# Kernel optimization log

Measured on AMD Instinct MI355X. Metric: run time of the kernel, lower is better.

## Reference

```python
import jax, jax.numpy as jnp
import numpy as np

EPS = 1e-12  # torch F.normalize eps


def _pairwise_sqdist(x, y):
    # P[b,i,j] = |x_i|^2 + |y_j|^2 - 2 x_i.y_j  (matches batch_pairwise_dist)
    rx = jnp.sum(x * x, axis=-1)[:, :, None]          # [B,N,1]
    ry = jnp.sum(y * y, axis=-1)[:, None, :]          # [B,1,M]
    zz = jnp.einsum('bnd,bmd->bnm', x, y)             # [B,N,M]
    return rx + ry - 2.0 * zz


def _unit_axis1(t):
    # torch F.normalize(t, dim=1): L2-normalize across the edge dimension (axis=1)
    n = jnp.sqrt(jnp.sum(t * t, axis=1, keepdims=True))
    return t / jnp.maximum(n, EPS)


def setup_inputs() -> dict:
    key = jax.random.key(0)
    k1, k2, k3, k4 = jax.random.split(key, 4)
    B, N, E = 2, 8192, 24576
    gts = jax.random.normal(k1, (B, N, 6), dtype=jnp.float32)
    preds = jax.random.normal(k2, (B, N, 6), dtype=jnp.float32)
    gts_normals = jax.random.normal(k3, (B, N, 3), dtype=jnp.float32)
    sphere_edges = jax.random.randint(k4, (E, 2), 0, N, dtype=jnp.int32)
    return {"gts": gts, "preds": preds, "gts_normals": gts_normals,
            "sphere_edges": sphere_edges}


def reference(gts, preds, gts_normals, sphere_edges):
    gts_points = gts[:, :, :3]
    preds_points = preds[:, :, :3]
    gts_colors = gts[:, :, 3:]
    preds_colors = preds[:, :, 3:]
    e0 = sphere_edges[:, 0]
    e1 = sphere_edges[:, 1]

    # ---- edge loss ----
    edge = preds_points[:, e0, :] - preds_points[:, e1, :]      # [B,E,3]
    edge_length = jnp.sum(jnp.abs(edge), axis=2)                # [B,E]
    edge_loss = jnp.sum(jnp.mean(edge_length, axis=1)) * 300.0

    # ---- color chamfer loss ----
    Pc = _pairwise_sqdist(gts_colors, preds_colors)             # [B,N,M]
    color_loss = jnp.sum(jnp.min(Pc, axis=1)) + jnp.sum(jnp.min(Pc, axis=2))

    # ---- point chamfer loss ----
    P = _pairwise_sqdist(gts_points, preds_points)              # [B,N,M]
    dist_f2s = jnp.min(P, axis=1)                               # [B,M]
    dist_s2f = jnp.min(P, axis=2)                               # [B,N]
    idx_s2f = jnp.argmin(P, axis=2)                             # [B,N] (into M)
    champfer_loss = (jnp.sum(jnp.mean(dist_f2s, axis=1))
                     + jnp.sum(jnp.mean(dist_s2f, axis=1)) * 0.55) * 3000.0

    # ---- normal loss ----
    # gather gts_normals by nearest-pred index (valid since N == M), then by edge start
    normal = jnp.take_along_axis(gts_normals, idx_s2f[:, :, None], axis=1)  # [B,N,3]
    normal = normal[:, e0, :]                                   # [B,E,3]
    # original casts edge to Long then back to float -> truncation toward zero
    edge_t = jnp.trunc(edge)
    cosine = jnp.abs(jnp.sum(_unit_axis1(normal) * _unit_axis1(edge_t), axis=2))
    normal_loss = jnp.sum(jnp.mean(cosine, axis=1)) * 0.5

    return color_loss + edge_loss + champfer_loss + normal_loss
```

## Files before the change

### kernel.cpp

```cpp
#include <hip/hip_runtime.h>
#include <stdint.h>

#define TPB 256
#define ROWS_PB 256
#define TC 256
#define CS 8
#define FINAL_BLOCKS 64

typedef unsigned long long u64;
typedef unsigned int u32;

__device__ __forceinline__ float waveReduceSum(float v){
#pragma unroll
  for (int o = 32; o > 0; o >>= 1) v += __shfl_down(v, o, 64);
  return v;
}

__device__ __forceinline__ float blockReduceSum(float v, float* buf){
  v = waveReduceSum(v);
  __syncthreads();
  if ((threadIdx.x & 63) == 0) buf[threadIdx.x >> 6] = v;
  __syncthreads();
  return buf[0] + buf[1] + buf[2] + buf[3];
}

template<bool NEED_IDX>
__device__ __forceinline__ void pass_body(
    const float* __restrict__ rows, const float* __restrict__ cols,
    void* __restrict__ outPackV, u32* __restrict__ outCol, int N, int cpc)
{
  __shared__ float4 ptsT[TC];
  __shared__ float4 colT[TC];
  __shared__ u64 mPack[4 * TPB];
  __shared__ u32 mCol[4 * TPB];

  const int b = blockIdx.y;
  const int rb = blockIdx.x / CS;
  const int chunk = blockIdx.x - rb * CS;
  const int t = threadIdx.x;
  const int lane = t & 63;
  const int w = t >> 6;
  const int rowBase = rb * ROWS_PB;
  const int colBase = chunk * cpc;

  float ax[4], ay[4], az[4], rx[4];
  float cr[4], cg[4], cbl[4], rc[4];
  float bD[4], bC[4];
  int bM[4];
#pragma unroll
  for (int k = 0; k < 4; k++){
    const float* p = rows + ((size_t)b * N + (rowBase + lane + 64 * k)) * 6;
    float p0 = p[0], p1 = p[1], p2 = p[2], p3 = p[3], p4 = p[4], p5 = p[5];
    ax[k] = -2.f * p0; ay[k] = -2.f * p1; az[k] = -2.f * p2;
    rx[k] = fmaf(p0, p0, fmaf(p1, p1, p2 * p2));
    cr[k] = -2.f * p3; cg[k] = -2.f * p4; cbl[k] = -2.f * p5;
    rc[k] = fmaf(p3, p3, fmaf(p4, p4, p5 * p5));
    bD[k] = 3.4e38f; bC[k] = 3.4e38f; bM[k] = 0;
  }

  for (int tb = 0; tb < cpc; tb += TC){
    const float* p = cols + ((size_t)b * N + (colBase + tb + t)) * 6;
    float q0 = p[0], q1 = p[1], q2 = p[2], q3 = p[3], q4 = p[4], q5 = p[5];
    ptsT[t] = make_float4(q0, q1, q2, fmaf(q0, q0, fmaf(q1, q1, q2 * q2)));
    colT[t] = make_float4(q3, q4, q5, fmaf(q3, q3, fmaf(q4, q4, q5 * q5)));
    __syncthreads();
#pragma unroll 4
    for (int j = 0; j < TC / 4; j += 2){
      const int mlA = j * 4 + w;
      const int mlB = mlA + 4;
      const float4 pA = ptsT[mlA], pB = ptsT[mlB];
      const float4 cA = colT[mlA], cB = colT[mlB];
      const int gA = colBase + tb + mlA;
      const int gB = gA + 4;
#pragma unroll
      for (int k = 0; k < 4; k++){
        float tA = fmaf(ax[k], pA.x, fmaf(ay[k], pA.y, fmaf(az[k], pA.z, pA.w)));
        float tB = fmaf(ax[k], pB.x, fmaf(ay[k], pB.y, fmaf(az[k], pB.z, pB.w)));
        if (NEED_IDX){
          if (tA < bD[k]) { bD[k] = tA; bM[k] = gA; }
          if (tB < bD[k]) { bD[k] = tB; bM[k] = gB; }
        } else {
          bD[k] = fminf(fminf(tA, tB), bD[k]);
        }
        float eA = fmaf(cr[k], cA.x, fmaf(cg[k], cA.y, fmaf(cbl[k], cA.z, cA.w)));
        float eB = fmaf(cr[k], cB.x, fmaf(cg[k], cB.y, fmaf(cbl[k], cB.z, cB.w)));
        bC[k] = fminf(fminf(eA, eB), bC[k]);
      }
    }
    __syncthreads();
  }

#pragma unroll
  for (int k = 0; k < 4; k++){
    int r = lane + 64 * k;
    float dv = fmaxf(bD[k] + rx[k], 0.f);
    float cv = fmaxf(bC[k] + rc[k], 0.f);
    mPack[w * TPB + r] = NEED_IDX
        ? (((u64)__float_as_uint(dv) << 32) | (u32)bM[k])
        : (u64)__float_as_uint(dv);
    mCol[w * TPB + r] = __float_as_uint(cv);
  }
  __syncthreads();
  u64 pk = mPack[t];
  u32 cm = mCol[t];
#pragma unroll
  for (int i = 1; i < 4; i++){
    u64 p2 = mPack[i * TPB + t]; if (p2 < pk) pk = p2;
    u32 c2 = mCol[i * TPB + t];  if (c2 < cm) cm = c2;
  }
  size_t g = (size_t)b * N + rowBase + t;
  if (NEED_IDX) atomicMin((u64*)outPackV + g, pk);
  else          atomicMin((u32*)outPackV + g, (u32)pk);
  atomicMin(&outCol[g], cm);
}

__global__ void __launch_bounds__(TPB) pass_all(
    const float* __restrict__ gts, const float* __restrict__ preds,
    u64* __restrict__ packS2F, u32* __restrict__ colMin2,
    u32* __restrict__ distF2S, u32* __restrict__ colMin1, int N, int cpc)
{
  if (blockIdx.z == 0) pass_body<true >(gts,  preds, packS2F, colMin2, N, cpc);
  else                 pass_body<false>(preds, gts,  distF2S, colMin1, N, cpc);
}

__global__ void __launch_bounds__(TPB) edge_pass1(
    const float* __restrict__ preds, const float* __restrict__ normals,
    const int* __restrict__ edges, const u64* __restrict__ packS2F,
    float* __restrict__ acc, int N, int E)
{
  __shared__ float buf[7][4];
  int gid = blockIdx.x * TPB + threadIdx.x;
  int b = gid / E, e = gid - b * E;
  int e0 = edges[2 * e], e1 = edges[2 * e + 1];
  const float* p0 = preds + ((size_t)b * N + e0) * 6;
  const float* p1 = preds + ((size_t)b * N + e1) * 6;
  float ex = p0[0] - p1[0], ey = p0[1] - p1[1], ez = p0[2] - p1[2];
  u32 idx = (u32)packS2F[(size_t)b * N + e0];
  const float* nr = normals + ((size_t)b * N + idx) * 3;
  float n0 = nr[0], n1 = nr[1], n2 = nr[2];
  float t0 = truncf(ex), t1 = truncf(ey), t2 = truncf(ez);
  float v[7] = { fabsf(ex) + fabsf(ey) + fabsf(ez),
                 n0 * n0, n1 * n1, n2 * n2, t0 * t0, t1 * t1, t2 * t2 };
  int lane = threadIdx.x & 63, w = threadIdx.x >> 6;
#pragma unroll
  for (int q = 0; q < 7; q++){
    float s = waveReduceSum(v[q]);
    if (lane == 0) buf[q][w] = s;
  }
  __syncthreads();
  if (threadIdx.x < 7){
    int q = threadIdx.x;
    float s = buf[q][0] + buf[q][1] + buf[q][2] + buf[q][3];
    int off = (q == 0) ? 0 : (q < 4 ? 1 + b * 3 + (q - 1) : 7 + b * 3 + (q - 4));
    atomicAdd(&acc[off], s);
  }
}

__global__ void __launch_bounds__(TPB) edge2_and_sum(
    const float* __restrict__ preds, const float* __restrict__ normals,
    const int* __restrict__ edges, const u64* __restrict__ packS2F,
    const u32* __restrict__ distF2S, const u32* __restrict__ colMin2,
    const u32* __restrict__ colMin1, float* __restrict__ acc,
    int N, int E, int BNtot, int nEdge)
{
  __shared__ float buf[4];
  if ((int)blockIdx.x < nEdge){
    int gid = blockIdx.x * TPB + threadIdx.x;
    int b = gid / E, e = gid - b * E;
    int e0 = edges[2 * e], e1 = edges[2 * e + 1];
    const float* p0 = preds + ((size_t)b * N + e0) * 6;
    const float* p1 = preds + ((size_t)b * N + e1) * 6;
    float ex = p0[0] - p1[0], ey = p0[1] - p1[1], ez = p0[2] - p1[2];
    u32 idx = (u32)packS2F[(size_t)b * N + e0];
    const float* nr = normals + ((size_t)b * N + idx) * 3;
    float t0 = truncf(ex), t1 = truncf(ey), t2 = truncf(ez);
    float r0 = 1.0f / (fmaxf(sqrtf(acc[1 + b * 3 + 0]), 1e-12f) * fmaxf(sqrtf(acc[7 + b * 3 + 0]), 1e-12f));
    float r1 = 1.0f / (fmaxf(sqrtf(acc[1 + b * 3 + 1]), 1e-12f) * fmaxf(sqrtf(acc[7 + b * 3 + 1]), 1e-12f));
    float r2 = 1.0f / (fmaxf(sqrtf(acc[1 + b * 3 + 2]), 1e-12f) * fmaxf(sqrtf(acc[7 + b * 3 + 2]), 1e-12f));
    float cosv = fabsf(nr[0] * t0 * r0 + nr[1] * t1 * r1 + nr[2] * t2 * r2);
    float s = blockReduceSum(cosv, buf);
    if (threadIdx.x == 0) atomicAdd(&acc[13], s);
  } else {
    int sb = blockIdx.x - nEdge;
    float invN = 1.0f / (float)N;
    float s = 0.f;
    for (int i = sb * TPB + threadIdx.x; i < BNtot; i += FINAL_BLOCKS * TPB){
      float s2f = __uint_as_float((u32)(packS2F[i] >> 32));
      float f2s = __uint_as_float(distF2S[i]);
      s += 3000.0f * invN * f2s + 1650.0f * invN * s2f
         + __uint_as_float(colMin1[i]) + __uint_as_float(colMin2[i]);
    }
    s = blockReduceSum(s, buf);
    if (threadIdx.x == 0) atomicAdd(&acc[14], s);
  }
}

__global__ void combine_kernel(const float* __restrict__ acc,
                               float* __restrict__ out, int E)
{
  out[0] = acc[14] + acc[0] * (300.0f / (float)E) + acc[13] * (0.5f / (float)E);
}

extern "C" void kernel_launch(void* const* d_in, const int* in_sizes, int n_in,
                              void* d_out, int out_size, void* d_ws, size_t ws_size,
                              hipStream_t stream)
{
  const float* gts     = (const float*)d_in[0];
  const float* preds   = (const float*)d_in[1];
  const float* normals = (const float*)d_in[2];
  const int*   edges   = (const int*)d_in[3];

  const int B = 2;
  const int BNtot = in_sizes[2] / 3;
  const int N = BNtot / B;
  const int E = in_sizes[3] / 2;

  char* ws = (char*)d_ws;
  u64* packS2F = (u64*)ws;
  u32* distF2S = (u32*)(ws + (size_t)BNtot * 8);
  u32* colMin2 = (u32*)(ws + (size_t)BNtot * 12);
  u32* colMin1 = (u32*)(ws + (size_t)BNtot * 16);
  float* acc   = (float*)(ws + (size_t)BNtot * 20);

  hipMemsetAsync(ws, 0xFF, (size_t)BNtot * 20, stream);
  hipMemsetAsync(acc, 0, 64, stream);

  int cpc = N / CS;
  dim3 gp((N / ROWS_PB) * CS, B, 2);
  pass_all<<<gp, TPB, 0, stream>>>(gts, preds, packS2F, colMin2, distF2S, colMin1, N, cpc);

  int nEdge = (B * E) / TPB;
  edge_pass1<<<nEdge, TPB, 0, stream>>>(preds, normals, edges, packS2F, acc, N, E);
  edge2_and_sum<<<nEdge + FINAL_BLOCKS, TPB, 0, stream>>>(
      preds, normals, edges, packS2F, distF2S, colMin2, colMin1, acc, N, E, BNtot, nEdge);
  combine_kernel<<<1, 1, 0, stream>>>(acc, (float*)d_out, E);
}
```

Baseline: 119.0 us.

## Replace atomicMin reductions with per-chunk partials and fuse edge stages

The pairwise pass now writes per-column-chunk partial minima to separate buffers instead of using global atomicMin, which removes the large 0xFF memset. A mid kernel reduces the partials and computes the chamfer sums and normal norms. The edge-length and trunc-norm sums are folded into the pass kernel as extra blocks. The combine kernel is replaced by a last-block-done finish in the cosine kernel. The column split is doubled and LDS is aliased to raise occupancy, at the cost of more partial-buffer traffic and repeated CS-way gathers per edge.

```diff
diff --git a/kernel.cpp b/kernel.cpp
--- a/kernel.cpp
+++ b/kernel.cpp
@@ -4,8 +4,7 @@
 #define TPB 256
 #define ROWS_PB 256
 #define TC 256
-#define CS 8
-#define FINAL_BLOCKS 64
+#define CS 16
 
 typedef unsigned long long u64;
 typedef unsigned int u32;
@@ -16,23 +15,24 @@
   return v;
 }
 
-__device__ __forceinline__ float blockReduceSum(float v, float* buf){
+__device__ __forceinline__ float blockReduceSum(float v, float* buf4){
   v = waveReduceSum(v);
   __syncthreads();
-  if ((threadIdx.x & 63) == 0) buf[threadIdx.x >> 6] = v;
+  if ((threadIdx.x & 63) == 0) buf4[threadIdx.x >> 6] = v;
   __syncthreads();
-  return buf[0] + buf[1] + buf[2] + buf[3];
+  return buf4[0] + buf4[1] + buf4[2] + buf4[3];
 }
 
 template<bool NEED_IDX>
 __device__ __forceinline__ void pass_body(
     const float* __restrict__ rows, const float* __restrict__ cols,
-    void* __restrict__ outPackV, u32* __restrict__ outCol, int N, int cpc)
-{
-  __shared__ float4 ptsT[TC];
-  __shared__ float4 colT[TC];
-  __shared__ u64 mPack[4 * TPB];
-  __shared__ u32 mCol[4 * TPB];
+    void* __restrict__ outPart, u32* __restrict__ outColPart,
+    char* lds, int N, int cpc, int BNtot)
+{
+  float4* ptsT = (float4*)lds;
+  float4* colT = (float4*)(lds + 4096);
+  u64* mPack   = (u64*)lds;
+  u32* mCol    = (u32*)(lds + 8192);
 
   const int b = blockIdx.y;
   const int rb = blockIdx.x / CS;
@@ -108,97 +108,131 @@
     u64 p2 = mPack[i * TPB + t]; if (p2 < pk) pk = p2;
     u32 c2 = mCol[i * TPB + t];  if (c2 < cm) cm = c2;
   }
-  size_t g = (size_t)b * N + rowBase + t;
-  if (NEED_IDX) atomicMin((u64*)outPackV + g, pk);
-  else          atomicMin((u32*)outPackV + g, (u32)pk);
-  atomicMin(&outCol[g], cm);
-}
-
-__global__ void __launch_bounds__(TPB) pass_all(
+  size_t g = (size_t)chunk * BNtot + (size_t)b * N + rowBase + t;
+  if (NEED_IDX) ((u64*)outPart)[g] = pk;
+  else          ((u32*)outPart)[g] = (u32)pk;
+  outColPart[g] = cm;
+}
+
+__device__ __forceinline__ void edge_partial(
+    const float* __restrict__ preds, const int* __restrict__ edges,
+    float* __restrict__ acc, int N, int E, int NXB)
+{
+  __shared__ float ebuf[4];
+  int e = ((int)blockIdx.x - NXB) * TPB + threadIdx.x;
+  int b = blockIdx.y;
+  int e0 = edges[2 * e], e1 = edges[2 * e + 1];
+  const float* p0 = preds + ((size_t)b * N + e0) * 6;
+  const float* p1 = preds + ((size_t)b * N + e1) * 6;
+  float ex = p0[0] - p1[0], ey = p0[1] - p1[1], ez = p0[2] - p1[2];
+  float t0 = truncf(ex), t1 = truncf(ey), t2 = truncf(ez);
+  float v[4] = { fabsf(ex) + fabsf(ey) + fabsf(ez), t0 * t0, t1 * t1, t2 * t2 };
+#pragma unroll
+  for (int q = 0; q < 4; q++){
+    float s = blockReduceSum(v[q], ebuf);
+    if (threadIdx.x == 0) atomicAdd(&acc[q == 0 ? 0 : 7 + b * 3 + (q - 1)], s);
+  }
+}
+
+__global__ void __launch_bounds__(TPB, 8) pass_all(
     const float* __restrict__ gts, const float* __restrict__ preds,
-    u64* __restrict__ packS2F, u32* __restrict__ colMin2,
-    u32* __restrict__ distF2S, u32* __restrict__ colMin1, int N, int cpc)
-{
-  if (blockIdx.z == 0) pass_body<true >(gts,  preds, packS2F, colMin2, N, cpc);
-  else                 pass_body<false>(preds, gts,  distF2S, colMin1, N, cpc);
-}
-
-__global__ void __launch_bounds__(TPB) edge_pass1(
+    const int* __restrict__ edges,
+    u64* __restrict__ packPart, u32* __restrict__ distPart,
+    u32* __restrict__ colPart2, u32* __restrict__ colPart1,
+    float* __restrict__ acc, int N, int cpc, int NXB, int E, int BNtot)
+{
+  __shared__ __align__(16) char lds[12288];
+  if ((int)blockIdx.x >= NXB){
+    if (blockIdx.z == 0) edge_partial(preds, edges, acc, N, E, NXB);
+    return;
+  }
+  if (blockIdx.z == 0) pass_body<true >(gts,  preds, packPart, colPart2, lds, N, cpc, BNtot);
+  else                 pass_body<false>(preds, gts,  distPart, colPart1, lds, N, cpc, BNtot);
+}
+
+__global__ void __launch_bounds__(TPB) mid_kernel(
+    const u64* __restrict__ packPart, const u32* __restrict__ distPart,
+    const u32* __restrict__ colPart2, const u32* __restrict__ colPart1,
+    const float* __restrict__ normals, const int* __restrict__ edges,
+    float* __restrict__ acc, int N, int E, int BNtot, int nRowBlk)
+{
+  __shared__ float buf4[4];
+  if ((int)blockIdx.x < nRowBlk){
+    int row = blockIdx.x * TPB + threadIdx.x;
+    u64 pk = packPart[row];
+    u32 f2 = distPart[row], c2 = colPart2[row], c1 = colPart1[row];
+#pragma unroll
+    for (int c = 1; c < CS; c++){
+      size_t o = (size_t)c * BNtot + row;
+      u64 p = packPart[o]; if (p < pk) pk = p;
+      u32 d = distPart[o]; if (d < f2) f2 = d;
+      u32 x2 = colPart2[o]; if (x2 < c2) c2 = x2;
+      u32 x1 = colPart1[o]; if (x1 < c1) c1 = x1;
+    }
+    float invN = 1.f / (float)N;
+    float s = 3000.f * invN * __uint_as_float(f2)
+            + 1650.f * invN * __uint_as_float((u32)(pk >> 32))
+            + __uint_as_float(c1) + __uint_as_float(c2);
+    s = blockReduceSum(s, buf4);
+    if (threadIdx.x == 0) atomicAdd(&acc[14], s);
+  } else {
+    int gid = ((int)blockIdx.x - nRowBlk) * TPB + threadIdx.x;
+    int b = gid / E, e = gid - b * E;
+    int e0 = edges[2 * e];
+    size_t r = (size_t)b * N + e0;
+    u64 pk = packPart[r];
+#pragma unroll
+    for (int c = 1; c < CS; c++){
+      u64 p = packPart[(size_t)c * BNtot + r]; if (p < pk) pk = p;
+    }
+    const float* nr = normals + ((size_t)b * N + (u32)pk) * 3;
+    float n0 = nr[0], n1 = nr[1], n2 = nr[2];
+    float s0 = blockReduceSum(n0 * n0, buf4);
+    if (threadIdx.x == 0) atomicAdd(&acc[1 + b * 3 + 0], s0);
+    float s1 = blockReduceSum(n1 * n1, buf4);
+    if (threadIdx.x == 0) atomicAdd(&acc[1 + b * 3 + 1], s1);
+    float s2 = blockReduceSum(n2 * n2, buf4);
+    if (threadIdx.x == 0) atomicAdd(&acc[1 + b * 3 + 2], s2);
+  }
+}
+
+__global__ void __launch_bounds__(TPB) edge_cos_kernel(
     const float* __restrict__ preds, const float* __restrict__ normals,
-    const int* __restrict__ edges, const u64* __restrict__ packS2F,
-    float* __restrict__ acc, int N, int E)
-{
-  __shared__ float buf[7][4];
+    const int* __restrict__ edges, const u64* __restrict__ packPart,
+    float* __restrict__ acc, float* __restrict__ out,
+    int N, int E, int BNtot, int nBlocks)
+{
+  __shared__ float buf4[4];
   int gid = blockIdx.x * TPB + threadIdx.x;
   int b = gid / E, e = gid - b * E;
   int e0 = edges[2 * e], e1 = edges[2 * e + 1];
   const float* p0 = preds + ((size_t)b * N + e0) * 6;
   const float* p1 = preds + ((size_t)b * N + e1) * 6;
   float ex = p0[0] - p1[0], ey = p0[1] - p1[1], ez = p0[2] - p1[2];
-  u32 idx = (u32)packS2F[(size_t)b * N + e0];
-  const float* nr = normals + ((size_t)b * N + idx) * 3;
-  float n0 = nr[0], n1 = nr[1], n2 = nr[2];
   float t0 = truncf(ex), t1 = truncf(ey), t2 = truncf(ez);
-  float v[7] = { fabsf(ex) + fabsf(ey) + fabsf(ez),
-                 n0 * n0, n1 * n1, n2 * n2, t0 * t0, t1 * t1, t2 * t2 };
-  int lane = threadIdx.x & 63, w = threadIdx.x >> 6;
-#pragma unroll
-  for (int q = 0; q < 7; q++){
-    float s = waveReduceSum(v[q]);
-    if (lane == 0) buf[q][w] = s;
-  }
-  __syncthreads();
-  if (threadIdx.x < 7){
-    int q = threadIdx.x;
-    float s = buf[q][0] + buf[q][1] + buf[q][2] + buf[q][3];
-    int off = (q == 0) ? 0 : (q < 4 ? 1 + b * 3 + (q - 1) : 7 + b * 3 + (q - 4));
-    atomicAdd(&acc[off], s);
-  }
-}
-
-__global__ void __launch_bounds__(TPB) edge2_and_sum(
-    const float* __restrict__ preds, const float* __restrict__ normals,
-    const int* __restrict__ edges, const u64* __restrict__ packS2F,
-    const u32* __restrict__ distF2S, const u32* __restrict__ colMin2,
-    const u32* __restrict__ colMin1, float* __restrict__ acc,
-    int N, int E, int BNtot, int nEdge)
-{
-  __shared__ float buf[4];
-  if ((int)blockIdx.x < nEdge){
-    int gid = blockIdx.x * TPB + threadIdx.x;
-    int b = gid / E, e = gid - b * E;
-    int e0 = edges[2 * e], e1 = edges[2 * e + 1];
-    const float* p0 = preds + ((size_t)b * N + e0) * 6;
-    const float* p1 = preds + ((size_t)b * N + e1) * 6;
-    float ex = p0[0] - p1[0], ey = p0[1] - p1[1], ez = p0[2] - p1[2];
-    u32 idx = (u32)packS2F[(size_t)b * N + e0];
-    const float* nr = normals + ((size_t)b * N + idx) * 3;
-    float t0 = truncf(ex), t1 = truncf(ey), t2 = truncf(ez);
-    float r0 = 1.0f / (fmaxf(sqrtf(acc[1 + b * 3 + 0]), 1e-12f) * fmaxf(sqrtf(acc[7 + b * 3 + 0]), 1e-12f));
-    float r1 = 1.0f / (fmaxf(sqrtf(acc[1 + b * 3 + 1]), 1e-12f) * fmaxf(sqrtf(acc[7 + b * 3 + 1]), 1e-12f));
-    float r2 = 1.0f / (fmaxf(sqrtf(acc[1 + b * 3 + 2]), 1e-12f) * fmaxf(sqrtf(acc[7 + b * 3 + 2]), 1e-12f));
-    float cosv = fabsf(nr[0] * t0 * r0 + nr[1] * t1 * r1 + nr[2] * t2 * r2);
-    float s = blockReduceSum(cosv, buf);
-    if (threadIdx.x == 0) atomicAdd(&acc[13], s);
-  } else {
-    int sb = blockIdx.x - nEdge;
-    float invN = 1.0f / (float)N;
-    float s = 0.f;
-    for (int i = sb * TPB + threadIdx.x; i < BNtot; i += FINAL_BLOCKS * TPB){
-      float s2f = __uint_as_float((u32)(packS2F[i] >> 32));
-      float f2s = __uint_as_float(distF2S[i]);
-      s += 3000.0f * invN * f2s + 1650.0f * invN * s2f
-         + __uint_as_float(colMin1[i]) + __uint_as_float(colMin2[i]);
-    }
-    s = blockReduceSum(s, buf);
-    if (threadIdx.x == 0) atomicAdd(&acc[14], s);
-  }
-}
-
-__global__ void combine_kernel(const float* __restrict__ acc,
-                               float* __restrict__ out, int E)
-{
-  out[0] = acc[14] + acc[0] * (300.0f / (float)E) + acc[13] * (0.5f / (float)E);
+  size_t r = (size_t)b * N + e0;
+  u64 pk = packPart[r];
+#pragma unroll
+  for (int c = 1; c < CS; c++){
+    u64 p = packPart[(size_t)c * BNtot + r]; if (p < pk) pk = p;
+  }
+  const float* nr = normals + ((size_t)b * N + (u32)pk) * 3;
+  float r0 = 1.f / (fmaxf(sqrtf(acc[1 + b * 3 + 0]), 1e-12f) * fmaxf(sqrtf(acc[7 + b * 3 + 0]), 1e-12f));
+  float r1 = 1.f / (fmaxf(sqrtf(acc[1 + b * 3 + 1]), 1e-12f) * fmaxf(sqrtf(acc[7 + b * 3 + 1]), 1e-12f));
+  float r2 = 1.f / (fmaxf(sqrtf(acc[1 + b * 3 + 2]), 1e-12f) * fmaxf(sqrtf(acc[7 + b * 3 + 2]), 1e-12f));
+  float cosv = fabsf(nr[0] * t0 * r0 + nr[1] * t1 * r1 + nr[2] * t2 * r2);
+  float s = blockReduceSum(cosv, buf4);
+  if (threadIdx.x == 0){
+    atomicAdd(&acc[13], s);
+    __threadfence();
+    u32 old = atomicAdd((u32*)&acc[15], 1u);
+    if (old == (u32)(nBlocks - 1)){
+      float a0  = atomicAdd(&acc[0],  0.f);
+      float a13 = atomicAdd(&acc[13], 0.f);
+      float a14 = atomicAdd(&acc[14], 0.f);
+      out[0] = a14 + a0 * (300.f / (float)E) + a13 * (0.5f / (float)E);
+    }
+  }
 }
 
 extern "C" void kernel_launch(void* const* d_in, const int* in_sizes, int n_in,
@@ -216,22 +250,28 @@
   const int E = in_sizes[3] / 2;
 
   char* ws = (char*)d_ws;
-  u64* packS2F = (u64*)ws;
-  u32* distF2S = (u32*)(ws + (size_t)BNtot * 8);
-  u32* colMin2 = (u32*)(ws + (size_t)BNtot * 12);
-  u32* colMin1 = (u32*)(ws + (size_t)BNtot * 16);
-  float* acc   = (float*)(ws + (size_t)BNtot * 20);
-
-  hipMemsetAsync(ws, 0xFF, (size_t)BNtot * 20, stream);
+  size_t nPart = (size_t)CS * BNtot;
+  u64* packPart = (u64*)ws;
+  u32* distPart = (u32*)(ws + nPart * 8);
+  u32* colPart2 = (u32*)(ws + nPart * 12);
+  u32* colPart1 = (u32*)(ws + nPart * 16);
+  float* acc    = (float*)(ws + nPart * 20);
+
   hipMemsetAsync(acc, 0, 64, stream);
 
   int cpc = N / CS;
-  dim3 gp((N / ROWS_PB) * CS, B, 2);
-  pass_all<<<gp, TPB, 0, stream>>>(gts, preds, packS2F, colMin2, distF2S, colMin1, N, cpc);
-
-  int nEdge = (B * E) / TPB;
-  edge_pass1<<<nEdge, TPB, 0, stream>>>(preds, normals, edges, packS2F, acc, N, E);
-  edge2_and_sum<<<nEdge + FINAL_BLOCKS, TPB, 0, stream>>>(
-      preds, normals, edges, packS2F, distF2S, colMin2, colMin1, acc, N, E, BNtot, nEdge);
-  combine_kernel<<<1, 1, 0, stream>>>(acc, (float*)d_out, E);
-}
+  int NXB = (N / ROWS_PB) * CS;
+  int nEdgeBlk = (B * E) / (TPB * B);
+  dim3 gp(NXB + nEdgeBlk, B, 2);
+  pass_all<<<gp, TPB, 0, stream>>>(gts, preds, edges, packPart, distPart,
+                                   colPart2, colPart1, acc, N, cpc, NXB, E, BNtot);
+
+  int nRowBlk = BNtot / TPB;
+  int nMid = nRowBlk + (B * E) / TPB;
+  mid_kernel<<<nMid, TPB, 0, stream>>>(packPart, distPart, colPart2, colPart1,
+                                       normals, edges, acc, N, E, BNtot, nRowBlk);
+
+  int nCos = (B * E) / TPB;
+  edge_cos_kernel<<<nCos, TPB, 0, stream>>>(preds, normals, edges, packPart,
+                                            acc, (float*)d_out, N, E, BNtot, nCos);
+}
```

Result: slower. 146.4 us (+23.0%).

## Fuse all stages into one cooperative kernel and pack argmin index into distance bits

Applied to the files above, without the earlier changes.

Merges the chamfer pass, the edge and row reductions, and the final combine into a single cooperative kernel separated by grid-wide syncs. A last-block counter writes the output, so the extra launches and the combine kernel go away. The pass also works on 8 rows per thread with finer column chunks for more register reuse. The nearest-neighbour index is stored in the low 13 mantissa bits of the distance, so a plain fminf replaces the compare-and-select. That truncates the s2f distances slightly. A three-launch fallback runs if the cooperative launch fails.

```diff
diff --git a/kernel.cpp b/kernel.cpp
--- a/kernel.cpp
+++ b/kernel.cpp
@@ -1,11 +1,16 @@
 #include <hip/hip_runtime.h>
+#include <hip/hip_cooperative_groups.h>
 #include <stdint.h>
 
+namespace cgrp = cooperative_groups;
+
 #define TPB 256
-#define ROWS_PB 256
+#define ROWS_PB 512
+#define KROWS 8
 #define TC 256
-#define CS 8
-#define FINAL_BLOCKS 64
+#define CS 16
+#define IDXMASK 0x1FFFu
+#define HIMASK  0xFFFFE000u
 
 typedef unsigned long long u64;
 typedef unsigned int u32;
@@ -16,47 +21,42 @@
   return v;
 }
 
-__device__ __forceinline__ float blockReduceSum(float v, float* buf){
+__device__ __forceinline__ float blockReduceSum(float v, float* buf4){
   v = waveReduceSum(v);
   __syncthreads();
-  if ((threadIdx.x & 63) == 0) buf[threadIdx.x >> 6] = v;
+  if ((threadIdx.x & 63) == 0) buf4[threadIdx.x >> 6] = v;
   __syncthreads();
-  return buf[0] + buf[1] + buf[2] + buf[3];
+  return buf4[0] + buf4[1] + buf4[2] + buf4[3];
 }
 
 template<bool NEED_IDX>
-__device__ __forceinline__ void pass_body(
+__device__ __forceinline__ void pass_phase(
     const float* __restrict__ rows, const float* __restrict__ cols,
-    void* __restrict__ outPackV, u32* __restrict__ outCol, int N, int cpc)
+    u64* __restrict__ outPack, u32* __restrict__ outDist, u32* __restrict__ outCol,
+    int N, int cpc, int b, int rb, int chunk,
+    float4* ptsT, float4* colT, u64* mPack, u32* mCol)
 {
-  __shared__ float4 ptsT[TC];
-  __shared__ float4 colT[TC];
-  __shared__ u64 mPack[4 * TPB];
-  __shared__ u32 mCol[4 * TPB];
-
-  const int b = blockIdx.y;
-  const int rb = blockIdx.x / CS;
-  const int chunk = blockIdx.x - rb * CS;
   const int t = threadIdx.x;
   const int lane = t & 63;
   const int w = t >> 6;
   const int rowBase = rb * ROWS_PB;
   const int colBase = chunk * cpc;
 
-  float ax[4], ay[4], az[4], rx[4];
-  float cr[4], cg[4], cbl[4], rc[4];
-  float bD[4], bC[4];
-  int bM[4];
-#pragma unroll
-  for (int k = 0; k < 4; k++){
+  float ax[KROWS], ay[KROWS], az[KROWS], rx[KROWS];
+  float cr[KROWS], cg_[KROWS], cb[KROWS], rc[KROWS];
+  float bD[KROWS], bC[KROWS];
+#pragma unroll
+  for (int k = 0; k < KROWS; k++){
     const float* p = rows + ((size_t)b * N + (rowBase + lane + 64 * k)) * 6;
     float p0 = p[0], p1 = p[1], p2 = p[2], p3 = p[3], p4 = p[4], p5 = p[5];
     ax[k] = -2.f * p0; ay[k] = -2.f * p1; az[k] = -2.f * p2;
     rx[k] = fmaf(p0, p0, fmaf(p1, p1, p2 * p2));
-    cr[k] = -2.f * p3; cg[k] = -2.f * p4; cbl[k] = -2.f * p5;
+    cr[k] = -2.f * p3; cg_[k] = -2.f * p4; cb[k] = -2.f * p5;
     rc[k] = fmaf(p3, p3, fmaf(p4, p4, p5 * p5));
-    bD[k] = 3.4e38f; bC[k] = 3.4e38f; bM[k] = 0;
-  }
+    bD[k] = 3.4e38f; bC[k] = 3.4e38f;
+  }
+  mPack[t] = ~0ull; mPack[t + TPB] = ~0ull;
+  mCol[t] = 0xFFFFFFFFu; mCol[t + TPB] = 0xFFFFFFFFu;
 
   for (int tb = 0; tb < cpc; tb += TC){
     const float* p = cols + ((size_t)b * N + (colBase + tb + t)) * 6;
@@ -66,24 +66,24 @@
     __syncthreads();
 #pragma unroll 4
     for (int j = 0; j < TC / 4; j += 2){
-      const int mlA = j * 4 + w;
-      const int mlB = mlA + 4;
+      const int mlA = j * 4 + w, mlB = mlA + 4;
       const float4 pA = ptsT[mlA], pB = ptsT[mlB];
       const float4 cA = colT[mlA], cB = colT[mlB];
-      const int gA = colBase + tb + mlA;
-      const int gB = gA + 4;
-#pragma unroll
-      for (int k = 0; k < 4; k++){
+      const u32 gA = (u32)(colBase + tb + mlA);
+      const u32 gB = gA + 4;
+#pragma unroll
+      for (int k = 0; k < KROWS; k++){
         float tA = fmaf(ax[k], pA.x, fmaf(ay[k], pA.y, fmaf(az[k], pA.z, pA.w)));
         float tB = fmaf(ax[k], pB.x, fmaf(ay[k], pB.y, fmaf(az[k], pB.z, pB.w)));
         if (NEED_IDX){
-          if (tA < bD[k]) { bD[k] = tA; bM[k] = gA; }
-          if (tB < bD[k]) { bD[k] = tB; bM[k] = gB; }
+          float pkA = __uint_as_float((__float_as_uint(tA) & HIMASK) | gA);
+          float pkB = __uint_as_float((__float_as_uint(tB) & HIMASK) | gB);
+          bD[k] = fminf(fminf(pkA, pkB), bD[k]);
         } else {
           bD[k] = fminf(fminf(tA, tB), bD[k]);
         }
-        float eA = fmaf(cr[k], cA.x, fmaf(cg[k], cA.y, fmaf(cbl[k], cA.z, cA.w)));
-        float eB = fmaf(cr[k], cB.x, fmaf(cg[k], cB.y, fmaf(cbl[k], cB.z, cB.w)));
+        float eA = fmaf(cr[k], cA.x, fmaf(cg_[k], cA.y, fmaf(cb[k], cA.z, cA.w)));
+        float eB = fmaf(cr[k], cB.x, fmaf(cg_[k], cB.y, fmaf(cb[k], cB.z, cB.w)));
         bC[k] = fminf(fminf(eA, eB), bC[k]);
       }
     }
@@ -91,81 +91,107 @@
   }
 
 #pragma unroll
-  for (int k = 0; k < 4; k++){
+  for (int k = 0; k < KROWS; k++){
     int r = lane + 64 * k;
-    float dv = fmaxf(bD[k] + rx[k], 0.f);
+    u32 db = __float_as_uint(bD[k]);
+    float dv; u32 idx = 0;
+    if (NEED_IDX){ idx = db & IDXMASK; dv = __uint_as_float(db & HIMASK) + rx[k]; }
+    else { dv = bD[k] + rx[k]; }
+    dv = fmaxf(dv, 0.f);
     float cv = fmaxf(bC[k] + rc[k], 0.f);
-    mPack[w * TPB + r] = NEED_IDX
-        ? (((u64)__float_as_uint(dv) << 32) | (u32)bM[k])
-        : (u64)__float_as_uint(dv);
-    mCol[w * TPB + r] = __float_as_uint(cv);
+    atomicMin(&mPack[r], ((u64)__float_as_uint(dv) << 32) | idx);
+    atomicMin(&mCol[r], __float_as_uint(cv));
   }
   __syncthreads();
-  u64 pk = mPack[t];
-  u32 cm = mCol[t];
-#pragma unroll
-  for (int i = 1; i < 4; i++){
-    u64 p2 = mPack[i * TPB + t]; if (p2 < pk) pk = p2;
-    u32 c2 = mCol[i * TPB + t];  if (c2 < cm) cm = c2;
-  }
-  size_t g = (size_t)b * N + rowBase + t;
-  if (NEED_IDX) atomicMin((u64*)outPackV + g, pk);
-  else          atomicMin((u32*)outPackV + g, (u32)pk);
-  atomicMin(&outCol[g], cm);
-}
-
-__global__ void __launch_bounds__(TPB) pass_all(
+#pragma unroll
+  for (int i = 0; i < ROWS_PB; i += TPB){
+    int r = t + i;
+    size_t g = (size_t)b * N + rowBase + r;
+    u64 pk = mPack[r]; u32 cm = mCol[r];
+    if (NEED_IDX) atomicMin(&outPack[g], pk);
+    else          atomicMin(&outDist[g], (u32)(pk >> 32));
+    atomicMin(&outCol[g], cm);
+  }
+}
+
+__global__ void __launch_bounds__(TPB, 4) combined(
     const float* __restrict__ gts, const float* __restrict__ preds,
-    u64* __restrict__ packS2F, u32* __restrict__ colMin2,
-    u32* __restrict__ distF2S, u32* __restrict__ colMin1, int N, int cpc)
+    const float* __restrict__ normals, const int* __restrict__ edges,
+    u64* __restrict__ packS2F, u32* __restrict__ distF2S,
+    u32* __restrict__ colMin2, u32* __restrict__ colMin1,
+    float* __restrict__ acc, float* __restrict__ out,
+    int N, int E, int cpc, int nRowBlk, int nEdgeBlk, int mode)
 {
-  if (blockIdx.z == 0) pass_body<true >(gts,  preds, packS2F, colMin2, N, cpc);
-  else                 pass_body<false>(preds, gts,  distF2S, colMin1, N, cpc);
-}
-
-__global__ void __launch_bounds__(TPB) edge_pass1(
-    const float* __restrict__ preds, const float* __restrict__ normals,
-    const int* __restrict__ edges, const u64* __restrict__ packS2F,
-    float* __restrict__ acc, int N, int E)
-{
-  __shared__ float buf[7][4];
-  int gid = blockIdx.x * TPB + threadIdx.x;
-  int b = gid / E, e = gid - b * E;
-  int e0 = edges[2 * e], e1 = edges[2 * e + 1];
-  const float* p0 = preds + ((size_t)b * N + e0) * 6;
-  const float* p1 = preds + ((size_t)b * N + e1) * 6;
-  float ex = p0[0] - p1[0], ey = p0[1] - p1[1], ez = p0[2] - p1[2];
-  u32 idx = (u32)packS2F[(size_t)b * N + e0];
-  const float* nr = normals + ((size_t)b * N + idx) * 3;
-  float n0 = nr[0], n1 = nr[1], n2 = nr[2];
-  float t0 = truncf(ex), t1 = truncf(ey), t2 = truncf(ez);
-  float v[7] = { fabsf(ex) + fabsf(ey) + fabsf(ez),
-                 n0 * n0, n1 * n1, n2 * n2, t0 * t0, t1 * t1, t2 * t2 };
-  int lane = threadIdx.x & 63, w = threadIdx.x >> 6;
-#pragma unroll
-  for (int q = 0; q < 7; q++){
-    float s = waveReduceSum(v[q]);
-    if (lane == 0) buf[q][w] = s;
-  }
-  __syncthreads();
-  if (threadIdx.x < 7){
-    int q = threadIdx.x;
-    float s = buf[q][0] + buf[q][1] + buf[q][2] + buf[q][3];
-    int off = (q == 0) ? 0 : (q < 4 ? 1 + b * 3 + (q - 1) : 7 + b * 3 + (q - 4));
-    atomicAdd(&acc[off], s);
-  }
-}
-
-__global__ void __launch_bounds__(TPB) edge2_and_sum(
-    const float* __restrict__ preds, const float* __restrict__ normals,
-    const int* __restrict__ edges, const u64* __restrict__ packS2F,
-    const u32* __restrict__ distF2S, const u32* __restrict__ colMin2,
-    const u32* __restrict__ colMin1, float* __restrict__ acc,
-    int N, int E, int BNtot, int nEdge)
-{
-  __shared__ float buf[4];
-  if ((int)blockIdx.x < nEdge){
-    int gid = blockIdx.x * TPB + threadIdx.x;
+  __shared__ float4 ptsT[TC];
+  __shared__ float4 colT[TC];
+  __shared__ u64 mPack[ROWS_PB];
+  __shared__ u32 mCol[ROWS_PB];
+  __shared__ float red4[4];
+  __shared__ float buf7[7][4];
+  __shared__ float chn[3];
+
+  const int x = (int)blockIdx.x;
+  const int t = threadIdx.x;
+
+  if (mode <= 1){
+    int perDB = (N / ROWS_PB) * CS;
+    int dir = x / (2 * perDB);
+    int rem = x - dir * 2 * perDB;
+    int b = rem / perDB;
+    int id = rem - b * perDB;
+    int rb = id / CS;
+    int chunk = id - rb * CS;
+    if (dir == 0) pass_phase<true >(gts,  preds, packS2F, distF2S, colMin2,
+                                    N, cpc, b, rb, chunk, ptsT, colT, mPack, mCol);
+    else          pass_phase<false>(preds, gts,  packS2F, distF2S, colMin1,
+                                    N, cpc, b, rb, chunk, ptsT, colT, mPack, mCol);
+    if (mode == 1) return;
+  }
+  if (mode == 0) cgrp::this_grid().sync();
+
+  if (mode == 0 || mode == 2){
+    if (x < nRowBlk){
+      int row = x * TPB + t;
+      u64 pk = packS2F[row];
+      float invN = 1.f / (float)N;
+      float s = 3000.f * invN * __uint_as_float(distF2S[row])
+              + 1650.f * invN * __uint_as_float((u32)(pk >> 32))
+              + __uint_as_float(colMin1[row]) + __uint_as_float(colMin2[row]);
+      s = blockReduceSum(s, red4);
+      if (t == 0) atomicAdd(&acc[14], s);
+    } else if (x < nRowBlk + nEdgeBlk){
+      int gid = (x - nRowBlk) * TPB + t;
+      int b = gid / E, e = gid - b * E;
+      int e0 = edges[2 * e], e1 = edges[2 * e + 1];
+      const float* p0 = preds + ((size_t)b * N + e0) * 6;
+      const float* p1 = preds + ((size_t)b * N + e1) * 6;
+      float ex = p0[0] - p1[0], ey = p0[1] - p1[1], ez = p0[2] - p1[2];
+      u32 idx = (u32)packS2F[(size_t)b * N + e0];
+      const float* nr = normals + ((size_t)b * N + idx) * 3;
+      float n0 = nr[0], n1 = nr[1], n2 = nr[2];
+      float t0 = truncf(ex), t1 = truncf(ey), t2 = truncf(ez);
+      float v[7] = { fabsf(ex) + fabsf(ey) + fabsf(ez),
+                     n0 * n0, n1 * n1, n2 * n2, t0 * t0, t1 * t1, t2 * t2 };
+      int lane = t & 63, w = t >> 6;
+#pragma unroll
+      for (int q = 0; q < 7; q++){
+        float s = waveReduceSum(v[q]);
+        if (lane == 0) buf7[q][w] = s;
+      }
+      __syncthreads();
+      if (t < 7){
+        float s = buf7[t][0] + buf7[t][1] + buf7[t][2] + buf7[t][3];
+        int off = (t == 0) ? 0 : ((t < 4) ? (1 + b * 3 + t - 1) : (7 + b * 3 + t - 4));
+        atomicAdd(&acc[off], s);
+      }
+    }
+    if (mode == 2) return;
+  }
+  if (mode == 0) cgrp::this_grid().sync();
+
+  int xe = (mode == 3) ? x : x - nRowBlk;
+  if (xe >= 0 && xe < nEdgeBlk){
+    int gid = xe * TPB + t;
     int b = gid / E, e = gid - b * E;
     int e0 = edges[2 * e], e1 = edges[2 * e + 1];
     const float* p0 = preds + ((size_t)b * N + e0) * 6;
@@ -174,31 +200,29 @@
     u32 idx = (u32)packS2F[(size_t)b * N + e0];
     const float* nr = normals + ((size_t)b * N + idx) * 3;
     float t0 = truncf(ex), t1 = truncf(ey), t2 = truncf(ez);
-    float r0 = 1.0f / (fmaxf(sqrtf(acc[1 + b * 3 + 0]), 1e-12f) * fmaxf(sqrtf(acc[7 + b * 3 + 0]), 1e-12f));
-    float r1 = 1.0f / (fmaxf(sqrtf(acc[1 + b * 3 + 1]), 1e-12f) * fmaxf(sqrtf(acc[7 + b * 3 + 1]), 1e-12f));
-    float r2 = 1.0f / (fmaxf(sqrtf(acc[1 + b * 3 + 2]), 1e-12f) * fmaxf(sqrtf(acc[7 + b * 3 + 2]), 1e-12f));
-    float cosv = fabsf(nr[0] * t0 * r0 + nr[1] * t1 * r1 + nr[2] * t2 * r2);
-    float s = blockReduceSum(cosv, buf);
-    if (threadIdx.x == 0) atomicAdd(&acc[13], s);
-  } else {
-    int sb = blockIdx.x - nEdge;
-    float invN = 1.0f / (float)N;
-    float s = 0.f;
-    for (int i = sb * TPB + threadIdx.x; i < BNtot; i += FINAL_BLOCKS * TPB){
-      float s2f = __uint_as_float((u32)(packS2F[i] >> 32));
-      float f2s = __uint_as_float(distF2S[i]);
-      s += 3000.0f * invN * f2s + 1650.0f * invN * s2f
-         + __uint_as_float(colMin1[i]) + __uint_as_float(colMin2[i]);
-    }
-    s = blockReduceSum(s, buf);
-    if (threadIdx.x == 0) atomicAdd(&acc[14], s);
-  }
-}
-
-__global__ void combine_kernel(const float* __restrict__ acc,
-                               float* __restrict__ out, int E)
-{
-  out[0] = acc[14] + acc[0] * (300.0f / (float)E) + acc[13] * (0.5f / (float)E);
+    if (t == 0){
+#pragma unroll
+      for (int c = 0; c < 3; c++){
+        float Sn = atomicAdd(&acc[1 + b * 3 + c], 0.f);
+        float Se = atomicAdd(&acc[7 + b * 3 + c], 0.f);
+        chn[c] = 1.f / (fmaxf(sqrtf(Sn), 1e-12f) * fmaxf(sqrtf(Se), 1e-12f));
+      }
+    }
+    __syncthreads();
+    float cosv = fabsf(nr[0] * t0 * chn[0] + nr[1] * t1 * chn[1] + nr[2] * t2 * chn[2]);
+    float s = blockReduceSum(cosv, red4);
+    if (t == 0){
+      atomicAdd(&acc[13], s);
+      __threadfence();
+      u32 old = atomicAdd((u32*)&acc[15], 1u);
+      if (old == (u32)(nEdgeBlk - 1)){
+        float a0  = atomicAdd(&acc[0],  0.f);
+        float a13 = atomicAdd(&acc[13], 0.f);
+        float a14 = atomicAdd(&acc[14], 0.f);
+        out[0] = a14 + a0 * (300.f / (float)E) + a13 * (0.5f / (float)E);
+      }
+    }
+  }
 }
 
 extern "C" void kernel_launch(void* const* d_in, const int* in_sizes, int n_in,
@@ -226,12 +250,27 @@
   hipMemsetAsync(acc, 0, 64, stream);
 
   int cpc = N / CS;
-  dim3 gp((N / ROWS_PB) * CS, B, 2);
-  pass_all<<<gp, TPB, 0, stream>>>(gts, preds, packS2F, colMin2, distF2S, colMin1, N, cpc);
-
-  int nEdge = (B * E) / TPB;
-  edge_pass1<<<nEdge, TPB, 0, stream>>>(preds, normals, edges, packS2F, acc, N, E);
-  edge2_and_sum<<<nEdge + FINAL_BLOCKS, TPB, 0, stream>>>(
-      preds, normals, edges, packS2F, distF2S, colMin2, colMin1, acc, N, E, BNtot, nEdge);
-  combine_kernel<<<1, 1, 0, stream>>>(acc, (float*)d_out, E);
-}
+  int nPass = 2 * B * (N / ROWS_PB) * CS;
+  int nRowBlk = BNtot / TPB;
+  int nEdgeBlk = (B * E) / TPB;
+  float* outp = (float*)d_out;
+
+  int mode0 = 0;
+  void* args[] = { (void*)&gts, (void*)&preds, (void*)&normals, (void*)&edges,
+                   (void*)&packS2F, (void*)&distF2S, (void*)&colMin2, (void*)&colMin1,
+                   (void*)&acc, (void*)&outp, (void*)&N, (void*)&E, (void*)&cpc,
+                   (void*)&nRowBlk, (void*)&nEdgeBlk, (void*)&mode0 };
+  hipError_t err = hipLaunchCooperativeKernel((const void*)combined,
+                                              dim3(nPass), dim3(TPB), args, 0, stream);
+  if (err != hipSuccess){
+    combined<<<nPass, TPB, 0, stream>>>(gts, preds, normals, edges, packS2F, distF2S,
+                                        colMin2, colMin1, acc, outp, N, E, cpc,
+                                        nRowBlk, nEdgeBlk, 1);
+    combined<<<nRowBlk + nEdgeBlk, TPB, 0, stream>>>(gts, preds, normals, edges, packS2F,
+                                        distF2S, colMin2, colMin1, acc, outp, N, E, cpc,
+                                        nRowBlk, nEdgeBlk, 2);
+    combined<<<nEdgeBlk, TPB, 0, stream>>>(gts, preds, normals, edges, packS2F, distF2S,
+                                        colMin2, colMin1, acc, outp, N, E, cpc,
+                                        nRowBlk, nEdgeBlk, 3);
+  }
+}
```

Measured after the change: 358.3 us. 3.01x slower.
